# Kernel optimization log

Measured on AMD Instinct MI355X. Metric: run time of the kernel, lower is better.

Reference implementation:

```python
import jax, jax.numpy as jnp
import numpy as np

B, S, HID = 2, 4096, 1024
NH, HD = 16, 64
R = 2  # dilation_rate


def setup_inputs() -> dict:
    key = jax.random.key(0)
    ks = jax.random.split(key, 6)
    sc = 0.02
    return {
        "hidden_states": jax.random.normal(ks[0], (B, S, HID), jnp.float32),
        "Wq": jax.random.normal(ks[1], (HID, HID), jnp.float32) * sc,
        "Wk": jax.random.normal(ks[2], (HID, HID), jnp.float32) * sc,
        "Wv": jax.random.normal(ks[3], (HID, HID), jnp.float32) * sc,
        "Wo": jax.random.normal(ks[4], (HID, HID), jnp.float32) * sc,
        "bo": jnp.zeros((HID,), jnp.float32),
    }


def reference(hidden_states, Wq, Wk, Wv, Wo, bo):
    bsz, q_len, _ = hidden_states.shape
    # projections (torch Linear: y = x @ W.T)
    q = jnp.einsum('bsh,oh->bso', hidden_states, Wq).reshape(bsz, q_len, NH, HD).transpose(0, 2, 1, 3)
    k = jnp.einsum('bsh,oh->bso', hidden_states, Wk).reshape(bsz, q_len, NH, HD).transpose(0, 2, 1, 3)
    v = jnp.einsum('bsh,oh->bso', hidden_states, Wv).reshape(bsz, q_len, NH, HD).transpose(0, 2, 1, 3)
    # strided dilation gather (indices 0, R, 2R, ...)
    q = q[:, :, ::R, :]
    k = k[:, :, ::R, :]
    v = v[:, :, ::R, :]
    sd = q.shape[2]  # dilated length
    # SDPA with is_causal=True over the dilated subsequence
    scores = jnp.einsum('bhqd,bhkd->bhqk', q, k) / np.sqrt(HD).astype(np.float32)
    causal = jnp.tril(jnp.ones((sd, sd), bool))
    scores = jnp.where(causal, scores, jnp.finfo(scores.dtype).min)
    probs = jax.nn.softmax(scores, axis=-1)
    attn = jnp.einsum('bhqk,bhkd->bhqd', probs, v)  # [B, H, sd, HD]
    attn = attn.transpose(0, 2, 1, 3).reshape(bsz, sd, HID)
    # scatter back into zero-initialized full-length tensor
    full = jnp.zeros((bsz, q_len, HID), attn.dtype).at[:, ::R, :].set(attn)
    return jnp.einsum('bsh,oh->bso', full, Wo) + bo
```

## Files before the change

kernel.cpp:

```cpp
#include <hip/hip_runtime.h>
#include <cstdint>

typedef unsigned short u16;
typedef unsigned int u32;
typedef __attribute__((ext_vector_type(8))) short short8;
typedef __attribute__((ext_vector_type(4))) float f32x4;
typedef __attribute__((ext_vector_type(4))) unsigned short u16x4;
typedef __attribute__((ext_vector_type(4))) u32 u32x4;
typedef __attribute__((ext_vector_type(2))) u32 u32x2;

#define S_ 4096
#define SD 2048

__device__ __forceinline__ u16 f2bf(float f) {
  union { float f; u32 u; } v; v.f = f;
  u32 r = v.u + 0x7fffu + ((v.u >> 16) & 1u);
  return (u16)(r >> 16);
}
#if __has_builtin(__builtin_amdgcn_cvt_pk_bf16_f32)
__device__ __forceinline__ u32 pkbf(float a, float b) {
  auto r = __builtin_amdgcn_cvt_pk_bf16_f32(a, b);
  u32 o; __builtin_memcpy(&o, &r, 4); return o;
}
#else
__device__ __forceinline__ u32 pkbf(float a, float b) {
  union { float f; u32 u; } ua, ub; ua.f = a; ub.f = b;
  return __builtin_amdgcn_perm(ub.u + 0x8000u, ua.u + 0x8000u, 0x07060302u);
}
#endif
__device__ __forceinline__ f32x4 mfma16(short8 a, short8 b, f32x4 c) {
  return __builtin_amdgcn_mfma_f32_16x16x32_bf16(a, b, c, 0, 0, 0);
}
__device__ __forceinline__ void async16(const void* g, void* l) {
  __builtin_amdgcn_global_load_lds((__attribute__((address_space(1))) void*)g,
                                   (__attribute__((address_space(3))) void*)l,
                                   16, 0, 0);
}

__global__ __launch_bounds__(256) void cast_all(const float* __restrict__ hs,
                                                const float* __restrict__ Wq,
                                                const float* __restrict__ Wk,
                                                const float* __restrict__ Wv,
                                                const float* __restrict__ Wo,
                                                u16* __restrict__ dstW,
                                                u16* __restrict__ dstX) {
  int bid = blockIdx.x;
  if (bid < 4096) {
    int gid = bid * 256 + threadIdx.x;
    int wsel = gid >> 18;
    int off  = (gid & 262143) * 4;
    const float* src = (wsel == 0) ? Wq : (wsel == 1) ? Wk : (wsel == 2) ? Wv : Wo;
    float scl = (wsel == 0) ? 0.18033688f : 1.0f;
    f32x4 v = *(const f32x4*)(src + off);
    u16x4 o; o.x = f2bf(v.x * scl); o.y = f2bf(v.y * scl);
    o.z = f2bf(v.z * scl); o.w = f2bf(v.w * scl);
    *(u16x4*)(dstW + (size_t)wsel * 1048576 + off) = o;
  } else {
    int gid = (bid - 4096) * 256 + threadIdx.x;
    int e = gid * 4;
    int m = e >> 10, col = e & 1023;
    int b = m >> 11, sm = m & 2047;
    const float* src = hs + ((size_t)(b * S_ + 2 * sm) << 10) + col;
    f32x4 v = *(const f32x4*)src;
    u16x4 o; o.x = f2bf(v.x); o.y = f2bf(v.y); o.z = f2bf(v.z); o.w = f2bf(v.w);
    *(u16x4*)(dstX + ((size_t)m << 10) + col) = o;
  }
}

__device__ __forceinline__ void gemm_body128(const u16* __restrict__ A,
                                             const u16* __restrict__ B,
                                             u16* __restrict__ C, int N,
                                             int bm, int bn, char* lA, char* lB) {
  const int tid = threadIdx.x, lane = tid & 63, w = tid >> 6;
  const int quad = lane >> 4, l15 = lane & 15;
  const int wm = (w & 1) * 64, wn = (w >> 1) * 64;
  f32x4 acc[4][4] = {};

  auto stage = [&](int buf, int k0) {
#pragma unroll
    for (int i = 0; i < 2; i++) {
      int p = i * 256 + tid;
      int row = p >> 2, cp = p & 3;
      int c = cp ^ ((row ^ (row >> 2)) & 3);
      async16(A + (size_t)(bm + row) * 1024 + k0 + c * 8,
              lA + buf * 8192 + i * 4096 + w * 1024);
      async16(B + (size_t)(bn + row) * 1024 + k0 + c * 8,
              lB + buf * 8192 + i * 4096 + w * 1024);
    }
  };

  stage(0, 0);
#pragma unroll 1
  for (int kt = 0; kt < 32; kt++) {
    __syncthreads();
    if (kt + 1 < 32) stage((kt + 1) & 1, (kt + 1) * 32);
    const char* A_ = lA + (kt & 1) * 8192;
    const char* B_ = lB + (kt & 1) * 8192;
    short8 af[4], bf[4];
#pragma unroll
    for (int mi = 0; mi < 4; mi++) {
      int row = wm + mi * 16 + l15;
      af[mi] = *(const short8*)(A_ + (row * 4 + (quad ^ ((row ^ (row >> 2)) & 3))) * 16);
    }
#pragma unroll
    for (int ni = 0; ni < 4; ni++) {
      int row = wn + ni * 16 + l15;
      bf[ni] = *(const short8*)(B_ + (row * 4 + (quad ^ ((row ^ (row >> 2)) & 3))) * 16);
    }
#pragma unroll
    for (int mi = 0; mi < 4; mi++)
#pragma unroll
      for (int ni = 0; ni < 4; ni++)
        acc[mi][ni] = mfma16(af[mi], bf[ni], acc[mi][ni]);
  }
#pragma unroll
  for (int mi = 0; mi < 4; mi++)
#pragma unroll
    for (int ni = 0; ni < 4; ni++) {
      int m0 = bm + wm + mi * 16 + quad * 4;
      int n = bn + wn + ni * 16 + l15;
#pragma unroll
      for (int r = 0; r < 4; r++)
        C[(size_t)(m0 + r) * N + n] = f2bf(acc[mi][ni][r]);
    }
}

__global__ __launch_bounds__(256) void qkv_gemm(const u16* __restrict__ X,
                                                const u16* __restrict__ Wbf,
                                                u16* __restrict__ QK,
                                                u16* __restrict__ Vt) {
  __shared__ __align__(16) char lA[16384];
  __shared__ __align__(16) char lB[16384];
  int bid = blockIdx.x;
  if (bid < 512) {
    gemm_body128(X, Wbf, QK, 2048, (bid >> 4) * 128, (bid & 15) * 128, lA, lB);
  } else {
    int b2 = bid - 512;
    gemm_body128(Wbf + 2 * 1048576, X, Vt, 4096, (b2 >> 5) * 128, (b2 & 31) * 128, lA, lB);
  }
}

__global__ __launch_bounds__(256) void oproj(const u16* __restrict__ A,
                                             const u16* __restrict__ B,
                                             const float* __restrict__ bo,
                                             float* __restrict__ out) {
  __shared__ __align__(16) char lA[8192];
  __shared__ __align__(16) char lB[16384];
  const int tid = threadIdx.x, lane = tid & 63, w = tid >> 6;
  const int quad = lane >> 4, l15 = lane & 15;
  const int bm = blockIdx.y * 64, bn = blockIdx.x * 128;
  const int wm = (w & 1) * 32, wn = (w >> 1) * 64;
  f32x4 acc[2][4] = {};

  auto stage = [&](int buf, int k0) {
    {
      int row = tid >> 2, cp = tid & 3;
      int c = cp ^ ((row ^ (row >> 2)) & 3);
      async16(A + (size_t)(bm + row) * 1024 + k0 + c * 8, lA + buf * 4096 + w * 1024);
    }
#pragma unroll
    for (int i = 0; i < 2; i++) {
      int p = i * 256 + tid;
      int row = p >> 2, cp = p & 3;
      int c = cp ^ ((row ^ (row >> 2)) & 3);
      async16(B + (size_t)(bn + row) * 1024 + k0 + c * 8, lB + buf * 8192 + i * 4096 + w * 1024);
    }
  };

  stage(0, 0);
#pragma unroll 1
  for (int kt = 0; kt < 32; kt++) {
    __syncthreads();
    if (kt + 1 < 32) stage((kt + 1) & 1, (kt + 1) * 32);
    const char* A_ = lA + (kt & 1) * 4096;
    const char* B_ = lB + (kt & 1) * 8192;
    short8 af[2], bf[4];
#pragma unroll
    for (int mi = 0; mi < 2; mi++) {
      int row = wm + mi * 16 + l15;
      af[mi] = *(const short8*)(A_ + (row * 4 + (quad ^ ((row ^ (row >> 2)) & 3))) * 16);
    }
#pragma unroll
    for (int ni = 0; ni < 4; ni++) {
      int row = wn + ni * 16 + l15;
      bf[ni] = *(const short8*)(B_ + (row * 4 + (quad ^ ((row ^ (row >> 2)) & 3))) * 16);
    }
#pragma unroll
    for (int mi = 0; mi < 2; mi++)
#pragma unroll
      for (int ni = 0; ni < 4; ni++)
        acc[mi][ni] = mfma16(af[mi], bf[ni], acc[mi][ni]);
  }
#pragma unroll
  for (int mi = 0; mi < 2; mi++)
#pragma unroll
    for (int ni = 0; ni < 4; ni++) {
      int n = bn + wn + ni * 16 + l15;
      float bias = bo[n];
#pragma unroll
      for (int r = 0; r < 4; r++) {
        int m = bm + wm + mi * 16 + quad * 4 + r;
        int bb = m >> 11, sm = m & 2047;
        size_t grow = ((size_t)(bb * S_ + 2 * sm)) << 10;
        out[grow + n] = acc[mi][ni][r] + bias;
        out[grow + 1024 + n] = bias;
      }
    }
}

__global__ __launch_bounds__(256) void attn6(const u16* __restrict__ QK,
                                             const u16* __restrict__ Vt,
                                             u16* __restrict__ O) {
  __shared__ __align__(16) char lK[2][8192];
  __shared__ __align__(16) char lV[2][8192];
  const int tid = threadIdx.x, lane = tid & 63, w = tid >> 6;
  const int quad = lane >> 4, l15 = lane & 15;
  const int h = blockIdx.x, b = blockIdx.y;
  const int qt = 31 - (int)blockIdx.z;
  const int qb = qt * 64 + w * 16;

  const u16* qp = QK + (size_t)(b * SD + qb + l15) * 2048 + h * 64 + quad * 8;
  short8 qf0 = *(const short8*)qp;
  short8 qf1 = *(const short8*)(qp + 32);

  auto stageK = [&](int buf, int kb) {
#pragma unroll
    for (int i = 0; i < 2; i++) {
      int p = (w * 2 + i) * 64 + lane;
      int row = p >> 3, c = (p & 7) ^ (row & 7);
      async16(QK + (size_t)(b * SD + kb + row) * 2048 + 1024 + h * 64 + c * 8,
              lK[buf] + (w * 2 + i) * 1024);
    }
  };

  const int vd = tid >> 2, vg = tid & 3;
  const u16* vgbase = Vt + (size_t)(h * 64 + vd) * 4096 + b * SD;
  const int vs = vd & 7;
  const int cb0 = (vg & 1) * 2;
  const int cb1 = cb0 + 4;
  const int inn = (vg >> 1) * 8;
  const int aw0 = vd * 128 + ((cb0     ^ vs) * 16) + inn;
  const int aw1 = vd * 128 + (((cb0+1) ^ vs) * 16) + inn;
  const int aw2 = vd * 128 + ((cb1     ^ vs) * 16) + inn;
  const int aw3 = vd * 128 + (((cb1+1) ^ vs) * 16) + inn;

  u32x4 nv0, nv1;
  auto loadV = [&](int kb) {
    nv0 = *(const u32x4*)(vgbase + kb + vg * 8);
    nv1 = *(const u32x4*)(vgbase + kb + 32 + vg * 8);
  };
  auto writeV = [&](int buf) {
    char* Vn = lV[buf];
    *(u32x2*)(Vn + aw0) = u32x2{nv0.x, nv0.y};
    *(u32x2*)(Vn + aw1) = u32x2{nv0.z, nv0.w};
    *(u32x2*)(Vn + aw2) = u32x2{nv1.x, nv1.y};
    *(u32x2*)(Vn + aw3) = u32x2{nv1.z, nv1.w};
  };

  f32x4 oacc[4] = {};
  float l4[4] = {0.f, 0.f, 0.f, 0.f};

  stageK(0, 0);
  loadV(0);
  writeV(0);

#pragma unroll 1
  for (int kt = 0; kt <= qt; kt++) {
    __syncthreads();
    if (kt + 1 <= qt) {
      stageK((kt + 1) & 1, (kt + 1) * 64);
      loadV((kt + 1) * 64);
    }
    const char* K_ = lK[kt & 1];
    const char* V_ = lV[kt & 1];

    f32x4 s[4];
#pragma unroll
    for (int m = 0; m < 4; m++) {
      int key = m * 16 + l15;
      short8 kf0 = *(const short8*)(K_ + (key * 8 + (quad ^ (key & 7))) * 16);
      short8 kf1 = *(const short8*)(K_ + (key * 8 + ((4 + quad) ^ (key & 7))) * 16);
      f32x4 a = {};
      a = mfma16(kf0, qf0, a);
      a = mfma16(kf1, qf1, a);
      s[m] = a;
    }
    if (kt == qt) {
      int qrel = w * 16 + l15;
#pragma unroll
      for (int m = 0; m < 4; m++)
#pragma unroll
        for (int r = 0; r < 4; r++)
          if (m * 16 + quad * 4 + r > qrel) s[m][r] = -1e30f;
    }
    float pr[4][4];
#pragma unroll
    for (int m = 0; m < 4; m++) {
#pragma unroll
      for (int r = 0; r < 4; r++) pr[m][r] = exp2f(s[m][r]);
      l4[m] += (pr[m][0] + pr[m][1]) + (pr[m][2] + pr[m][3]);
    }
    u32 pw[8];
#pragma unroll
    for (int m = 0; m < 4; m++) {
      pw[m * 2]     = pkbf(pr[m][0], pr[m][1]);
      pw[m * 2 + 1] = pkbf(pr[m][2], pr[m][3]);
    }
    short8 pf0, pf1;
    __builtin_memcpy(&pf0, &pw[0], 16);
    __builtin_memcpy(&pf1, &pw[4], 16);

#pragma unroll
    for (int m = 0; m < 4; m++) {
      int dr = m * 16 + l15;
      short8 vf0 = *(const short8*)(V_ + (dr * 128 + ((quad     ^ (dr & 7)) * 16)));
      short8 vf1 = *(const short8*)(V_ + (dr * 128 + (((4+quad) ^ (dr & 7)) * 16)));
      oacc[m] = mfma16(vf0, pf0, oacc[m]);
      oacc[m] = mfma16(vf1, pf1, oacc[m]);
    }
    if (kt + 1 <= qt) writeV((kt + 1) & 1);
  }

  float l = (l4[0] + l4[1]) + (l4[2] + l4[3]);
  l += __shfl_xor(l, 16, 64);
  l += __shfl_xor(l, 32, 64);
  float inv = 1.0f / l;
  u16* op = O + (size_t)(b * SD + qb + l15) * 1024 + h * 64;
#pragma unroll
  for (int m = 0; m < 4; m++) {
    u16x4 ov;
#pragma unroll
    for (int r = 0; r < 4; r++) ov[r] = f2bf(oacc[m][r] * inv);
    *(u16x4*)(op + m * 16 + quad * 4) = ov;
  }
}

extern "C" void kernel_launch(void* const* d_in, const int* in_sizes, int n_in,
                              void* d_out, int out_size, void* d_ws, size_t ws_size,
                              hipStream_t stream) {
  (void)in_sizes; (void)n_in; (void)out_size; (void)ws_size;
  const float* hs = (const float*)d_in[0];
  const float* Wq = (const float*)d_in[1];
  const float* Wk = (const float*)d_in[2];
  const float* Wv = (const float*)d_in[3];
  const float* Wo = (const float*)d_in[4];
  const float* bo = (const float*)d_in[5];
  float* out = (float*)d_out;
  char* ws = (char*)d_ws;

  u16* Xbf = (u16*)ws;
  u16* Wbf = (u16*)(ws + (8u << 20));
  u16* QKb = (u16*)(ws + (16u << 20));
  u16* Vtb = (u16*)(ws + (32u << 20));
  u16* Ob  = (u16*)(ws + (40u << 20));

  cast_all<<<8192, 256, 0, stream>>>(hs, Wq, Wk, Wv, Wo, Wbf, Xbf);
  qkv_gemm<<<768, 256, 0, stream>>>(Xbf, Wbf, QKb, Vtb);
  attn6<<<dim3(16, 2, 32), 256, 0, stream>>>(QKb, Vtb, Ob);
  oproj<<<dim3(8, 64), 256, 0, stream>>>(Ob, Wbf + 3 * 1048576, bo, out);
}
```

Measured before the change: 190.7 us.

## Give each attention wave two query sub-tiles to reuse K/V fragments

The attention kernel drops from four waves per block to two. Each wave now handles 32 query rows as two 16-row MFMA sub-tiles, so every K and V fragment read from LDS feeds twice as many MFMAs. The code that stages K and V is reworked so 128 threads fill the same 64-key tiles. In exchange each wave holds more registers (two accumulator sets), and blocks have fewer waves to hide latency; launch_bounds(128,3) is meant to keep occupancy up.

```diff
diff --git a/kernel.cpp b/kernel.cpp
--- a/kernel.cpp
+++ b/kernel.cpp
@@ -208,57 +208,67 @@
     }
 }
 
-__global__ __launch_bounds__(256) void attn6(const u16* __restrict__ QK,
-                                             const u16* __restrict__ Vt,
-                                             u16* __restrict__ O) {
+__global__ __launch_bounds__(128, 3) void attn7(const u16* __restrict__ QK,
+                                                const u16* __restrict__ Vt,
+                                                u16* __restrict__ O) {
   __shared__ __align__(16) char lK[2][8192];
   __shared__ __align__(16) char lV[2][8192];
   const int tid = threadIdx.x, lane = tid & 63, w = tid >> 6;
   const int quad = lane >> 4, l15 = lane & 15;
   const int h = blockIdx.x, b = blockIdx.y;
   const int qt = 31 - (int)blockIdx.z;
-  const int qb = qt * 64 + w * 16;
-
-  const u16* qp = QK + (size_t)(b * SD + qb + l15) * 2048 + h * 64 + quad * 8;
-  short8 qf0 = *(const short8*)qp;
-  short8 qf1 = *(const short8*)(qp + 32);
+  const int qb = qt * 64 + w * 32;
+
+  short8 qf[2][2];
+#pragma unroll
+  for (int n = 0; n < 2; n++) {
+    const u16* qp = QK + (size_t)(b * SD + qb + n * 16 + l15) * 2048 + h * 64 + quad * 8;
+    qf[n][0] = *(const short8*)qp;
+    qf[n][1] = *(const short8*)(qp + 32);
+  }
 
   auto stageK = [&](int buf, int kb) {
 #pragma unroll
-    for (int i = 0; i < 2; i++) {
-      int p = (w * 2 + i) * 64 + lane;
+    for (int i = 0; i < 4; i++) {
+      int p = (w * 4 + i) * 64 + lane;
       int row = p >> 3, c = (p & 7) ^ (row & 7);
       async16(QK + (size_t)(b * SD + kb + row) * 2048 + 1024 + h * 64 + c * 8,
-              lK[buf] + (w * 2 + i) * 1024);
-    }
-  };
-
-  const int vd = tid >> 2, vg = tid & 3;
+              lK[buf] + (w * 4 + i) * 1024);
+    }
+  };
+
+  const int vd = tid >> 1, g = tid & 1;
   const u16* vgbase = Vt + (size_t)(h * 64 + vd) * 4096 + b * SD;
   const int vs = vd & 7;
-  const int cb0 = (vg & 1) * 2;
-  const int cb1 = cb0 + 4;
-  const int inn = (vg >> 1) * 8;
-  const int aw0 = vd * 128 + ((cb0     ^ vs) * 16) + inn;
-  const int aw1 = vd * 128 + (((cb0+1) ^ vs) * 16) + inn;
-  const int aw2 = vd * 128 + ((cb1     ^ vs) * 16) + inn;
-  const int aw3 = vd * 128 + (((cb1+1) ^ vs) * 16) + inn;
-
-  u32x4 nv0, nv1;
+  int aw[8];
+#pragma unroll
+  for (int j = 0; j < 4; j++) {
+    int G = g + 2 * j;
+#pragma unroll
+    for (int s = 0; s < 2; s++) {
+      int q = 2 * G + s;
+      aw[j * 2 + s] = vd * 128 + (((q & 3) + 4 * (q >> 3)) ^ vs) * 16 + ((q >> 2) & 1) * 8;
+    }
+  }
+
+  u32x4 nv[4];
   auto loadV = [&](int kb) {
-    nv0 = *(const u32x4*)(vgbase + kb + vg * 8);
-    nv1 = *(const u32x4*)(vgbase + kb + 32 + vg * 8);
+#pragma unroll
+    for (int j = 0; j < 4; j++)
+      nv[j] = *(const u32x4*)(vgbase + kb + (g + 2 * j) * 8);
   };
   auto writeV = [&](int buf) {
     char* Vn = lV[buf];
-    *(u32x2*)(Vn + aw0) = u32x2{nv0.x, nv0.y};
-    *(u32x2*)(Vn + aw1) = u32x2{nv0.z, nv0.w};
-    *(u32x2*)(Vn + aw2) = u32x2{nv1.x, nv1.y};
-    *(u32x2*)(Vn + aw3) = u32x2{nv1.z, nv1.w};
-  };
-
-  f32x4 oacc[4] = {};
-  float l4[4] = {0.f, 0.f, 0.f, 0.f};
+#pragma unroll
+    for (int j = 0; j < 4; j++) {
+      *(u32x2*)(Vn + aw[j * 2])     = u32x2{nv[j].x, nv[j].y};
+      *(u32x2*)(Vn + aw[j * 2 + 1]) = u32x2{nv[j].z, nv[j].w};
+    }
+  };
+
+  f32x4 oacc[2][4] = {};
+  f32x4 l4v[2] = {};
+  const f32x4 zf = {};
 
   stageK(0, 0);
   loadV(0);
@@ -273,65 +283,67 @@
     }
     const char* K_ = lK[kt & 1];
     const char* V_ = lV[kt & 1];
-
-    f32x4 s[4];
+    const bool last = (kt == qt);
+
+    u32 pw[2][8];
 #pragma unroll
     for (int m = 0; m < 4; m++) {
       int key = m * 16 + l15;
       short8 kf0 = *(const short8*)(K_ + (key * 8 + (quad ^ (key & 7))) * 16);
       short8 kf1 = *(const short8*)(K_ + (key * 8 + ((4 + quad) ^ (key & 7))) * 16);
-      f32x4 a = {};
-      a = mfma16(kf0, qf0, a);
-      a = mfma16(kf1, qf1, a);
-      s[m] = a;
-    }
-    if (kt == qt) {
-      int qrel = w * 16 + l15;
-#pragma unroll
-      for (int m = 0; m < 4; m++)
-#pragma unroll
-        for (int r = 0; r < 4; r++)
-          if (m * 16 + quad * 4 + r > qrel) s[m][r] = -1e30f;
-    }
-    float pr[4][4];
-#pragma unroll
-    for (int m = 0; m < 4; m++) {
-#pragma unroll
-      for (int r = 0; r < 4; r++) pr[m][r] = exp2f(s[m][r]);
-      l4[m] += (pr[m][0] + pr[m][1]) + (pr[m][2] + pr[m][3]);
-    }
-    u32 pw[8];
-#pragma unroll
-    for (int m = 0; m < 4; m++) {
-      pw[m * 2]     = pkbf(pr[m][0], pr[m][1]);
-      pw[m * 2 + 1] = pkbf(pr[m][2], pr[m][3]);
-    }
-    short8 pf0, pf1;
-    __builtin_memcpy(&pf0, &pw[0], 16);
-    __builtin_memcpy(&pf1, &pw[4], 16);
+#pragma unroll
+      for (int n = 0; n < 2; n++) {
+        f32x4 a = mfma16(kf0, qf[n][0], zf);
+        a = mfma16(kf1, qf[n][1], a);
+        if (last) {
+          int qrel = w * 32 + n * 16 + l15;
+#pragma unroll
+          for (int r = 0; r < 4; r++)
+            if (m * 16 + quad * 4 + r > qrel) a[r] = -1e30f;
+        }
+        f32x4 p;
+#pragma unroll
+        for (int r = 0; r < 4; r++) p[r] = exp2f(a[r]);
+        l4v[n] += p;
+        pw[n][m * 2]     = pkbf(p[0], p[1]);
+        pw[n][m * 2 + 1] = pkbf(p[2], p[3]);
+      }
+    }
+    short8 pf[2][2];
+#pragma unroll
+    for (int n = 0; n < 2; n++) {
+      __builtin_memcpy(&pf[n][0], &pw[n][0], 16);
+      __builtin_memcpy(&pf[n][1], &pw[n][4], 16);
+    }
 
 #pragma unroll
     for (int m = 0; m < 4; m++) {
       int dr = m * 16 + l15;
       short8 vf0 = *(const short8*)(V_ + (dr * 128 + ((quad     ^ (dr & 7)) * 16)));
       short8 vf1 = *(const short8*)(V_ + (dr * 128 + (((4+quad) ^ (dr & 7)) * 16)));
-      oacc[m] = mfma16(vf0, pf0, oacc[m]);
-      oacc[m] = mfma16(vf1, pf1, oacc[m]);
+#pragma unroll
+      for (int n = 0; n < 2; n++) {
+        oacc[n][m] = mfma16(vf0, pf[n][0], oacc[n][m]);
+        oacc[n][m] = mfma16(vf1, pf[n][1], oacc[n][m]);
+      }
     }
     if (kt + 1 <= qt) writeV((kt + 1) & 1);
   }
 
-  float l = (l4[0] + l4[1]) + (l4[2] + l4[3]);
-  l += __shfl_xor(l, 16, 64);
-  l += __shfl_xor(l, 32, 64);
-  float inv = 1.0f / l;
-  u16* op = O + (size_t)(b * SD + qb + l15) * 1024 + h * 64;
-#pragma unroll
-  for (int m = 0; m < 4; m++) {
-    u16x4 ov;
-#pragma unroll
-    for (int r = 0; r < 4; r++) ov[r] = f2bf(oacc[m][r] * inv);
-    *(u16x4*)(op + m * 16 + quad * 4) = ov;
+#pragma unroll
+  for (int n = 0; n < 2; n++) {
+    float l = (l4v[n][0] + l4v[n][1]) + (l4v[n][2] + l4v[n][3]);
+    l += __shfl_xor(l, 16, 64);
+    l += __shfl_xor(l, 32, 64);
+    float inv = 1.0f / l;
+    u16* op = O + (size_t)(b * SD + qb + n * 16 + l15) * 1024 + h * 64;
+#pragma unroll
+    for (int m = 0; m < 4; m++) {
+      u16x4 ov;
+#pragma unroll
+      for (int r = 0; r < 4; r++) ov[r] = f2bf(oacc[n][m][r] * inv);
+      *(u16x4*)(op + m * 16 + quad * 4) = ov;
+    }
   }
 }
 
@@ -356,6 +368,6 @@
 
   cast_all<<<8192, 256, 0, stream>>>(hs, Wq, Wk, Wv, Wo, Wbf, Xbf);
   qkv_gemm<<<768, 256, 0, stream>>>(Xbf, Wbf, QKb, Vtb);
-  attn6<<<dim3(16, 2, 32), 256, 0, stream>>>(QKb, Vtb, Ob);
+  attn7<<<dim3(16, 2, 32), 128, 0, stream>>>(QKb, Vtb, Ob);
   oproj<<<dim3(8, 64), 256, 0, stream>>>(Ob, Wbf + 3 * 1048576, bo, out);
 }
```

After: 211.1 us. +10.7%, slower.

## Split long causal query tiles' KV range across two blocks with a combine pass

Applied to the files above, without the earlier changes.

Query tiles in the upper half of the sequence now run as two blocks, each covering half of the key range. Chunk 0 writes unnormalized fp32 partials and chunk 1 writes bf16 partials, each with its row sums. A new combine kernel adds the partials, normalizes them and writes bf16 output. The goal is to balance causal-attention work across more blocks, at the cost of an extra launch, extra partial-buffer traffic, and reduced precision in the bf16 partial.

```diff
diff --git a/kernel.cpp b/kernel.cpp
--- a/kernel.cpp
+++ b/kernel.cpp
@@ -16,6 +16,9 @@
   union { float f; u32 u; } v; v.f = f;
   u32 r = v.u + 0x7fffu + ((v.u >> 16) & 1u);
   return (u16)(r >> 16);
+}
+__device__ __forceinline__ float bf2f(u16 x) {
+  union { u32 u; float f; } v; v.u = ((u32)x) << 16; return v.f;
 }
 #if __has_builtin(__builtin_amdgcn_cvt_pk_bf16_f32)
 __device__ __forceinline__ u32 pkbf(float a, float b) {
@@ -208,15 +211,26 @@
     }
 }
 
-__global__ __launch_bounds__(256) void attn6(const u16* __restrict__ QK,
+__global__ __launch_bounds__(256) void attn8(const u16* __restrict__ QK,
                                              const u16* __restrict__ Vt,
-                                             u16* __restrict__ O) {
+                                             u16* __restrict__ O,
+                                             float* __restrict__ Op0,
+                                             u16* __restrict__ Op1,
+                                             float* __restrict__ lp) {
   __shared__ __align__(16) char lK[2][8192];
   __shared__ __align__(16) char lV[2][8192];
   const int tid = threadIdx.x, lane = tid & 63, w = tid >> 6;
   const int quad = lane >> 4, l15 = lane & 15;
   const int h = blockIdx.x, b = blockIdx.y;
-  const int qt = 31 - (int)blockIdx.z;
+  const int z = (int)blockIdx.z;
+  int qt, chunk, c0, c1;
+  if (z < 32) {
+    qt = 31 - (z >> 1); chunk = z & 1;
+    if (chunk == 0) { c0 = 0; c1 = 15; } else { c0 = 16; c1 = qt; }
+  } else {
+    qt = 47 - z; chunk = 0; c0 = 0; c1 = qt;
+  }
+  const bool par = (z < 32);
   const int qb = qt * 64 + w * 16;
 
   const u16* qp = QK + (size_t)(b * SD + qb + l15) * 2048 + h * 64 + quad * 8;
@@ -260,14 +274,14 @@
   f32x4 oacc[4] = {};
   float l4[4] = {0.f, 0.f, 0.f, 0.f};
 
-  stageK(0, 0);
-  loadV(0);
+  stageK(0, c0 * 64);
+  loadV(c0 * 64);
   writeV(0);
 
 #pragma unroll 1
-  for (int kt = 0; kt <= qt; kt++) {
+  for (int kt = c0; kt <= c1; kt++) {
     __syncthreads();
-    if (kt + 1 <= qt) {
+    if (kt + 1 <= c1) {
       stageK((kt + 1) & 1, (kt + 1) * 64);
       loadV((kt + 1) * 64);
     }
@@ -318,21 +332,63 @@
       oacc[m] = mfma16(vf0, pf0, oacc[m]);
       oacc[m] = mfma16(vf1, pf1, oacc[m]);
     }
-    if (kt + 1 <= qt) writeV((kt + 1) & 1);
+    if (kt + 1 <= c1) writeV((kt + 1) & 1);
   }
 
   float l = (l4[0] + l4[1]) + (l4[2] + l4[3]);
   l += __shfl_xor(l, 16, 64);
   l += __shfl_xor(l, 32, 64);
+
+  if (!par) {
+    float inv = 1.0f / l;
+    u16* op = O + (size_t)(b * SD + qb + l15) * 1024 + h * 64;
+#pragma unroll
+    for (int m = 0; m < 4; m++) {
+      u16x4 ov;
+#pragma unroll
+      for (int r = 0; r < 4; r++) ov[r] = f2bf(oacc[m][r] * inv);
+      *(u16x4*)(op + m * 16 + quad * 4) = ov;
+    }
+  } else {
+    int rq = b * 1024 + (qb - 1024 + l15);
+    if (chunk == 0) {
+      float* p0 = Op0 + ((size_t)rq << 10) + h * 64 + quad * 4;
+#pragma unroll
+      for (int m = 0; m < 4; m++)
+        *(f32x4*)(p0 + m * 16) = oacc[m];
+    } else {
+      u16* p1 = Op1 + ((size_t)rq << 10) + h * 64 + quad * 4;
+#pragma unroll
+      for (int m = 0; m < 4; m++) {
+        u16x4 ov;
+#pragma unroll
+        for (int r = 0; r < 4; r++) ov[r] = f2bf(oacc[m][r]);
+        *(u16x4*)(p1 + m * 16) = ov;
+      }
+    }
+    if (quad == 0) lp[chunk * 32768 + rq * 16 + h] = l;
+  }
+}
+
+__global__ __launch_bounds__(256) void combine_po(const float* __restrict__ Op0,
+                                                  const u16* __restrict__ Op1,
+                                                  const float* __restrict__ lp,
+                                                  u16* __restrict__ O) {
+  int gid = blockIdx.x * 256 + threadIdx.x;
+  int row = gid >> 8;
+  int d0 = (gid & 255) * 4;
+  int hh = d0 >> 6;
+  float l = lp[row * 16 + hh] + lp[32768 + row * 16 + hh];
   float inv = 1.0f / l;
-  u16* op = O + (size_t)(b * SD + qb + l15) * 1024 + h * 64;
-#pragma unroll
-  for (int m = 0; m < 4; m++) {
-    u16x4 ov;
-#pragma unroll
-    for (int r = 0; r < 4; r++) ov[r] = f2bf(oacc[m][r] * inv);
-    *(u16x4*)(op + m * 16 + quad * 4) = ov;
-  }
+  f32x4 a = *(const f32x4*)(Op0 + ((size_t)row << 10) + d0);
+  u16x4 b1 = *(const u16x4*)(Op1 + ((size_t)row << 10) + d0);
+  int bb = row >> 10, qr = row & 1023;
+  u16* op = O + ((size_t)(bb * SD + 1024 + qr) << 10) + d0;
+  u16x4 o;
+#pragma unroll
+  for (int r = 0; r < 4; r++)
+    o[r] = f2bf((a[r] + bf2f(b1[r])) * inv);
+  *(u16x4*)op = o;
 }
 
 extern "C" void kernel_launch(void* const* d_in, const int* in_sizes, int n_in,
@@ -354,8 +410,13 @@
   u16* Vtb = (u16*)(ws + (32u << 20));
   u16* Ob  = (u16*)(ws + (40u << 20));
 
+  float* Op0 = (float*)ws;
+  float* lp  = (float*)(ws + (8u << 20));
+  u16*   Op1 = (u16*)(ws + (9u << 20));
+
   cast_all<<<8192, 256, 0, stream>>>(hs, Wq, Wk, Wv, Wo, Wbf, Xbf);
   qkv_gemm<<<768, 256, 0, stream>>>(Xbf, Wbf, QKb, Vtb);
-  attn6<<<dim3(16, 2, 32), 256, 0, stream>>>(QKb, Vtb, Ob);
+  attn8<<<dim3(16, 2, 48), 256, 0, stream>>>(QKb, Vtb, Ob, Op0, Op1, lp);
+  combine_po<<<2048, 256, 0, stream>>>(Op0, Op1, lp, Ob);
   oproj<<<dim3(8, 64), 256, 0, stream>>>(Ob, Wbf + 3 * 1048576, bo, out);
 }
```

Result: slower. 197.3 us (+3.5%).
